# Optimization experiments

Measured on AMD Instinct MI355X. Metric: run time of the kernel, lower is better.

Reference implementation:

```python
import jax, jax.numpy as jnp
import numpy as np

B, S_CTX, S_Q, D_CTX, D_Q = 16, 2048, 2048, 1024, 1024
MASK_P = 0.1  # fraction of masked context positions


def setup_inputs() -> dict:
    key = jax.random.key(0)
    k1, k2, k3, k4 = jax.random.split(key, 4)
    context = jax.random.normal(k1, (B, S_CTX, D_CTX), dtype=jnp.float32)
    query = jax.random.normal(k2, (S_Q, B, D_Q), dtype=jnp.float32)  # [q_steps, batch, query_size]
    W = jax.random.normal(k3, (D_CTX, D_Q), dtype=jnp.float32)       # learned bilinear weights
    context_mask = jax.random.uniform(k4, (B, S_CTX)) < MASK_P       # True = masked position
    return {"context": context, "query": query, "W": W, "context_mask": context_mask}


def reference(context, query, W, context_mask):
    # scores[b, q, s] = context[b, s, :] @ W @ query[q, b, :]   (temp = 1.0, so no scaling)
    cw = jnp.einsum('bsd,de->bse', context, W)            # [B, S_ctx, D_q]
    scores = jnp.einsum('bse,qbe->bqs', cw, query)        # [B, S_q, S_ctx]
    neg = jnp.asarray(-1e30, scores.dtype)                # finite stand-in for -inf (NaN-safe)
    scores = jnp.where(context_mask[:, None, :], neg, scores)
    attn = jax.nn.softmax(scores, axis=2)                 # [B, S_q, S_ctx]
    # rows where the whole context is masked get attention zeroed out
    all_masked = jnp.all(context_mask, axis=1)[:, None, None]
    attn = jnp.where(all_masked, jnp.asarray(0.0, attn.dtype), attn)
    composition = jnp.einsum('bqs,bsd->qbd', attn, context)  # [S_q, B, D_ctx]
    attn_out = attn.transpose(1, 0, 2)                       # [S_q, B, S_ctx]
    return attn_out, composition
```

## Files before the change

kernel.cpp:

```cpp
#include <hip/hip_runtime.h>
#include <cmath>

#define B_  16
#define SEQ 2048
#define DIM 1024
#define LDST 40

typedef short  short8 __attribute__((ext_vector_type(8)));
typedef short  sh4    __attribute__((ext_vector_type(4)));
typedef float  f32x4  __attribute__((ext_vector_type(4)));

__device__ __forceinline__ unsigned short f2bf(float x) {
  unsigned u = __builtin_bit_cast(unsigned, x);
  return (unsigned short)((u + 0x7fffu + ((u >> 16) & 1u)) >> 16);
}
__device__ __forceinline__ float bf2f(unsigned short h) {
  unsigned u = ((unsigned)h) << 16;
  return __builtin_bit_cast(float, u);
}

__device__ __forceinline__ void gl16(const void* g, void* l) {
  __builtin_amdgcn_global_load_lds(
      (const __attribute__((address_space(1))) void*)g,
      (__attribute__((address_space(3))) void*)l, 16, 0, 0);
}

__global__ __launch_bounds__(256) void cvt_ctx(const float* __restrict__ X,
                                               unsigned short* __restrict__ hi,
                                               unsigned short* __restrict__ lo) {
  const size_t N8 = (size_t)B_ * SEQ * DIM / 8;
  for (size_t i = (size_t)blockIdx.x * 256 + threadIdx.x; i < N8;
       i += (size_t)gridDim.x * 256) {
    const size_t base = i * 8;
    float4 a = *(const float4*)&X[base];
    float4 c = *(const float4*)&X[base + 4];
    const float xs[8] = {a.x, a.y, a.z, a.w, c.x, c.y, c.z, c.w};
    short8 h, l;
#pragma unroll
    for (int j = 0; j < 8; ++j) {
      unsigned short hh = f2bf(xs[j]);
      h[j] = (short)hh;
      l[j] = (short)f2bf(xs[j] - bf2f(hh));
    }
    *(short8*)&hi[base] = h;
    *(short8*)&lo[base] = l;
  }
}

__global__ __launch_bounds__(256) void t_ctx(const float* __restrict__ X,
                                             unsigned short* __restrict__ T) {
  __shared__ unsigned short L[64 * 72];
  const int t = threadIdx.x;
  const int d0 = blockIdx.x * 64, s0 = blockIdx.y * 64, b = blockIdx.z;
#pragma unroll
  for (int p = 0; p < 4; ++p) {
    const int sl = (t >> 4) + p * 16, d4 = (t & 15) * 4;
    float4 v = *(const float4*)&X[((size_t)b * SEQ + s0 + sl) * DIM + d0 + d4];
    sh4 o = {(short)f2bf(v.x), (short)f2bf(v.y), (short)f2bf(v.z), (short)f2bf(v.w)};
    *(sh4*)&L[sl * 72 + d4] = o;
  }
  __syncthreads();
#pragma unroll
  for (int p = 0; p < 4; ++p) {
    const int dl = (t >> 4) + p * 16, s4 = (t & 15) * 4;
    sh4 o = {(short)L[(s4 + 0) * 72 + dl], (short)L[(s4 + 1) * 72 + dl],
             (short)L[(s4 + 2) * 72 + dl], (short)L[(s4 + 3) * 72 + dl]};
    *(sh4*)&T[((size_t)b * DIM + d0 + dl) * SEQ + s0 + s4] = o;
  }
}

__global__ __launch_bounds__(256) void g1_z(const float* __restrict__ Q,
                                            const float* __restrict__ W,
                                            unsigned short* __restrict__ zhi,
                                            unsigned short* __restrict__ zlo) {
  __shared__ unsigned short Ah[128 * LDST], Al[128 * LDST];
  __shared__ unsigned short Bh[128 * LDST], Bl[128 * LDST];
  const int tid = threadIdx.x;
  const int m0 = blockIdx.y * 128, n0 = blockIdx.x * 128;
  const int wave = tid >> 6, lane = tid & 63;
  const int wm = (wave >> 1) * 64, wn = (wave & 1) * 64;
  const int rl = tid & 127;

  const float* srow = (tid < 128) ? Q + (size_t)(m0 + rl) * DIM
                                  : W + (size_t)(n0 + rl) * DIM;
  unsigned short* th = (tid < 128) ? Ah : Bh;
  unsigned short* tl = (tid < 128) ? Al : Bl;

  f32x4 acc[4][4];
#pragma unroll
  for (int i = 0; i < 4; ++i)
#pragma unroll
    for (int j = 0; j < 4; ++j) acc[i][j] = (f32x4){0.f, 0.f, 0.f, 0.f};

  for (int kc = 0; kc < DIM; kc += 32) {
    float4 fv[8];
#pragma unroll
    for (int j = 0; j < 8; ++j) fv[j] = *(const float4*)&srow[kc + j * 4];
    __syncthreads();
    short8 hv[4], lv[4];
#pragma unroll
    for (int j = 0; j < 8; ++j) {
      const float x[4] = {fv[j].x, fv[j].y, fv[j].z, fv[j].w};
#pragma unroll
      for (int c = 0; c < 4; ++c) {
        unsigned short h = f2bf(x[c]);
        unsigned short l = f2bf(x[c] - bf2f(h));
        hv[j >> 1][(j & 1) * 4 + c] = (short)h;
        lv[j >> 1][(j & 1) * 4 + c] = (short)l;
      }
    }
#pragma unroll
    for (int j = 0; j < 4; ++j) {
      *(short8*)&th[rl * LDST + j * 8] = hv[j];
      *(short8*)&tl[rl * LDST + j * 8] = lv[j];
    }
    __syncthreads();

    short8 ah[4], al[4], bh[4], bl[4];
#pragma unroll
    for (int f = 0; f < 4; ++f) {
      const int ao = (wm + f * 16 + (lane & 15)) * LDST + (lane >> 4) * 8;
      const int bo = (wn + f * 16 + (lane & 15)) * LDST + (lane >> 4) * 8;
      ah[f] = *(const short8*)&Ah[ao];  al[f] = *(const short8*)&Al[ao];
      bh[f] = *(const short8*)&Bh[bo];  bl[f] = *(const short8*)&Bl[bo];
    }
#pragma unroll
    for (int i = 0; i < 4; ++i)
#pragma unroll
      for (int j = 0; j < 4; ++j) {
        acc[i][j] = __builtin_amdgcn_mfma_f32_16x16x32_bf16(ah[i], bh[j], acc[i][j], 0, 0, 0);
        acc[i][j] = __builtin_amdgcn_mfma_f32_16x16x32_bf16(al[i], bh[j], acc[i][j], 0, 0, 0);
        acc[i][j] = __builtin_amdgcn_mfma_f32_16x16x32_bf16(ah[i], bl[j], acc[i][j], 0, 0, 0);
      }
  }
#pragma unroll
  for (int i = 0; i < 4; ++i)
#pragma unroll
    for (int j = 0; j < 4; ++j)
#pragma unroll
      for (int r = 0; r < 4; ++r) {
        const int row = m0 + wm + i * 16 + (lane >> 4) * 4 + r;
        const int col = n0 + wn + j * 16 + (lane & 15);
        const float v = acc[i][j][r];
        const unsigned short h = f2bf(v);
        zhi[(size_t)row * DIM + col] = h;
        zlo[(size_t)row * DIM + col] = f2bf(v - bf2f(h));
      }
}

#define G2GRID (16 * 16 * B_)
__global__ __launch_bounds__(256) void g2_scores(const unsigned short* __restrict__ zhi,
                                                 const unsigned short* __restrict__ zlo,
                                                 const unsigned short* __restrict__ chi,
                                                 const unsigned short* __restrict__ clo,
                                                 float* __restrict__ Sc) {
  __shared__ unsigned short Sh[128 * 32], Sl[128 * 32];
  __shared__ unsigned short Qh[128 * 32], Ql[128 * 32];
  const int tid = threadIdx.x, lane = tid & 63, wave = tid >> 6;

  const int lin = blockIdx.x;
  const int swz = (lin & 7) * (G2GRID / 8) + (lin >> 3);
  const int s0 = (swz & 15) * 128;
  const int q0 = ((swz >> 4) & 15) * 128;
  const int b  = swz >> 8;

  const int wm = (wave >> 1) * 64;
  const int wn = (wave & 1) * 64;

  const int r_sub = lane >> 2;
  const int c_sub = (((lane & 3) ^ ((lane >> 3) & 3))) * 8;

  f32x4 acc[4][4];
#pragma unroll
  for (int i = 0; i < 4; ++i)
#pragma unroll
    for (int j = 0; j < 4; ++j) acc[i][j] = (f32x4){0.f, 0.f, 0.f, 0.f};

  for (int kc = 0; kc < DIM; kc += 32) {
    if (wave == 0) {
#pragma unroll
      for (int it = 0; it < 8; ++it)
        gl16(&chi[((size_t)b * SEQ + s0 + it * 16 + r_sub) * DIM + kc + c_sub], &Sh[it * 512]);
    } else if (wave == 1) {
#pragma unroll
      for (int it = 0; it < 8; ++it)
        gl16(&clo[((size_t)b * SEQ + s0 + it * 16 + r_sub) * DIM + kc + c_sub], &Sl[it * 512]);
    } else if (wave == 2) {
#pragma unroll
      for (int it = 0; it < 8; ++it)
        gl16(&zhi[((size_t)(q0 + it * 16 + r_sub) * B_ + b) * DIM + kc + c_sub], &Qh[it * 512]);
    } else {
#pragma unroll
      for (int it = 0; it < 8; ++it)
        gl16(&zlo[((size_t)(q0 + it * 16 + r_sub) * B_ + b) * DIM + kc + c_sub], &Ql[it * 512]);
    }
    __syncthreads();

    short8 sh_[4], sl_[4], qh_[4], ql_[4];
#pragma unroll
    for (int f = 0; f < 4; ++f) {
      const int ra = wm + f * 16 + (lane & 15);
      const int rb = wn + f * 16 + (lane & 15);
      const int so = ra * 32 + (((lane >> 4) ^ ((ra >> 1) & 3))) * 8;
      const int qo = rb * 32 + (((lane >> 4) ^ ((rb >> 1) & 3))) * 8;
      sh_[f] = *(const short8*)&Sh[so];  sl_[f] = *(const short8*)&Sl[so];
      qh_[f] = *(const short8*)&Qh[qo];  ql_[f] = *(const short8*)&Ql[qo];
    }
#pragma unroll
    for (int i = 0; i < 4; ++i)
#pragma unroll
      for (int j = 0; j < 4; ++j) {
        acc[i][j] = __builtin_amdgcn_mfma_f32_16x16x32_bf16(sh_[i], qh_[j], acc[i][j], 0, 0, 0);
        acc[i][j] = __builtin_amdgcn_mfma_f32_16x16x32_bf16(sl_[i], qh_[j], acc[i][j], 0, 0, 0);
        acc[i][j] = __builtin_amdgcn_mfma_f32_16x16x32_bf16(sh_[i], ql_[j], acc[i][j], 0, 0, 0);
      }
    __syncthreads();
  }

#pragma unroll
  for (int i = 0; i < 4; ++i)
#pragma unroll
    for (int j = 0; j < 4; ++j) {
      const int s = s0 + wm + i * 16 + (lane >> 4) * 4;
      const int q = q0 + wn + j * 16 + (lane & 15);
      f32x4 v = {acc[i][j][0], acc[i][j][1], acc[i][j][2], acc[i][j][3]};
      __builtin_nontemporal_store(v, (f32x4*)&Sc[((size_t)q * B_ + b) * SEQ + s]);
    }
}

__global__ __launch_bounds__(256) void kernel_softmax(float* __restrict__ attn,
                                                      const int* __restrict__ mask) {
  const int row = blockIdx.x;
  const int b = row & (B_ - 1);
  float* p = attn + (size_t)row * SEQ;
  const int* m = mask + (size_t)b * SEQ;
  const int t = threadIdx.x;

  float v[8];
  float mx = -INFINITY;
#pragma unroll
  for (int i = 0; i < 8; ++i) {
    const int s = t + i * 256;
    float x = p[s];
    x = m[s] ? -1e30f : x;
    v[i] = x;
    mx = fmaxf(mx, x);
  }
#pragma unroll
  for (int off = 32; off > 0; off >>= 1) mx = fmaxf(mx, __shfl_xor(mx, off));
  __shared__ float redmax[4];
  __shared__ float redsum[4];
  if ((t & 63) == 0) redmax[t >> 6] = mx;
  __syncthreads();
  mx = fmaxf(fmaxf(redmax[0], redmax[1]), fmaxf(redmax[2], redmax[3]));

  float sum = 0.f;
#pragma unroll
  for (int i = 0; i < 8; ++i) {
    v[i] = __expf(v[i] - mx);
    sum += v[i];
  }
#pragma unroll
  for (int off = 32; off > 0; off >>= 1) sum += __shfl_xor(sum, off);
  if ((t & 63) == 0) redsum[t >> 6] = sum;
  __syncthreads();
  sum = (redsum[0] + redsum[1]) + (redsum[2] + redsum[3]);

  const bool allmasked = (mx < -1e29f);
  const float inv = allmasked ? 0.f : 1.f / sum;
#pragma unroll
  for (int i = 0; i < 8; ++i) p[t + i * 256] = v[i] * inv;
}

__global__ __launch_bounds__(256) void g3_comp(const float* __restrict__ attn,
                                               const unsigned short* __restrict__ ctxT,
                                               float* __restrict__ Out) {
  __shared__ unsigned short Ad[128 * 32];
  __shared__ unsigned short Bq[128 * 32];
  const int tid = threadIdx.x, lane = tid & 63, wave = tid >> 6;
  const int b = blockIdx.z;
  const int d0 = blockIdx.x * 128, q0 = blockIdx.y * 128;
  const int wm = (wave >> 1) * 64;
  const int wn = (wave & 1) * 64;

  const int r_sub = lane >> 2;
  const int c_sub = (((lane & 3) ^ ((lane >> 3) & 3))) * 8;

  const int qrow = tid >> 1, shalf = (tid & 1) * 16;
  const float* arow = attn + ((size_t)(q0 + qrow) * B_ + b) * SEQ;
  const int qsw = (qrow >> 1) & 3;
  const int blk_base = (tid & 1) * 2;
  unsigned short* bdst0 = &Bq[qrow * 32 + ((blk_base + 0) ^ qsw) * 8];
  unsigned short* bdst1 = &Bq[qrow * 32 + ((blk_base + 1) ^ qsw) * 8];

  f32x4 acc[4][4];
#pragma unroll
  for (int i = 0; i < 4; ++i)
#pragma unroll
    for (int j = 0; j < 4; ++j) acc[i][j] = (f32x4){0.f, 0.f, 0.f, 0.f};

  for (int kc = 0; kc < SEQ; kc += 32) {
    float4 fv[4];
#pragma unroll
    for (int j = 0; j < 4; ++j) fv[j] = *(const float4*)&arow[kc + shalf + j * 4];
#pragma unroll
    for (int i = 0; i < 2; ++i) {
      const int rb = wave * 32 + i * 16;
      gl16(&ctxT[((size_t)b * DIM + d0 + rb + r_sub) * SEQ + kc + c_sub], &Ad[rb * 32]);
    }
    short8 bv0, bv1;
#pragma unroll
    for (int j = 0; j < 4; ++j) {
      const float x[4] = {fv[j].x, fv[j].y, fv[j].z, fv[j].w};
#pragma unroll
      for (int c = 0; c < 4; ++c) {
        const int e = j * 4 + c;
        if (e < 8) bv0[e] = (short)f2bf(x[c]);
        else       bv1[e - 8] = (short)f2bf(x[c]);
      }
    }
    *(short8*)bdst0 = bv0;
    *(short8*)bdst1 = bv1;
    __syncthreads();

    short8 af[4], bf_[4];
#pragma unroll
    for (int f = 0; f < 4; ++f) {
      const int ra = wm + f * 16 + (lane & 15);
      const int rb = wn + f * 16 + (lane & 15);
      af[f]  = *(const short8*)&Ad[ra * 32 + (((lane >> 4) ^ ((ra >> 1) & 3))) * 8];
      bf_[f] = *(const short8*)&Bq[rb * 32 + (((lane >> 4) ^ ((rb >> 1) & 3))) * 8];
    }
#pragma unroll
    for (int i = 0; i < 4; ++i)
#pragma unroll
      for (int j = 0; j < 4; ++j)
        acc[i][j] = __builtin_amdgcn_mfma_f32_16x16x32_bf16(af[i], bf_[j], acc[i][j], 0, 0, 0);
    __syncthreads();
  }

#pragma unroll
  for (int i = 0; i < 4; ++i)
#pragma unroll
    for (int j = 0; j < 4; ++j) {
      const int d = d0 + wm + i * 16 + (lane >> 4) * 4;
      const int q = q0 + wn + j * 16 + (lane & 15);
      f32x4 v = {acc[i][j][0], acc[i][j][1], acc[i][j][2], acc[i][j][3]};
      __builtin_nontemporal_store(v, (f32x4*)&Out[((size_t)q * B_ + b) * DIM + d]);
    }
}

extern "C" void kernel_launch(void* const* d_in, const int* in_sizes, int n_in,
                              void* d_out, int out_size, void* d_ws, size_t ws_size,
                              hipStream_t stream) {
  const float* context = (const float*)d_in[0];
  const float* query   = (const float*)d_in[1];
  const float* W       = (const float*)d_in[2];
  const int*   mask    = (const int*)d_in[3];

  float* attn = (float*)d_out;
  float* comp = attn + (size_t)SEQ * B_ * SEQ;

  unsigned short* chi = (unsigned short*)comp;
  unsigned short* clo = chi + (size_t)B_ * SEQ * DIM;

  unsigned short* zhi  = (unsigned short*)d_ws;
  unsigned short* zlo  = zhi + (size_t)SEQ * B_ * DIM;
  unsigned short* ctxT = (unsigned short*)d_ws;

  cvt_ctx<<<dim3(4096), 256, 0, stream>>>(context, chi, clo);
  g1_z<<<dim3(DIM / 128, (SEQ * B_) / 128), 256, 0, stream>>>(query, W, zhi, zlo);
  g2_scores<<<dim3(G2GRID), 256, 0, stream>>>(zhi, zlo, chi, clo, attn);
  t_ctx<<<dim3(DIM / 64, SEQ / 64, B_), 256, 0, stream>>>(context, ctxT);
  kernel_softmax<<<dim3(SEQ * B_), 256, 0, stream>>>(attn, mask);
  g3_comp<<<dim3(DIM / 128, SEQ / 128, B_), 256, 0, stream>>>(attn, ctxT, comp);
}
```

Baseline: 1.258 ms.

## Widen composition K-tile to 64, vectorize softmax, transpose from bf16 hi buffer

The composition GEMM now stages a 64-wide K slice per iteration with an 8-way XOR swizzle, which halves the number of barrier-separated iterations and doubles the MFMAs issued per sync. The softmax kernel switches from strided scalar accesses to contiguous float4/int4 loads and stores per thread. The context transpose now reads the already converted bf16 hi buffer instead of the fp32 context, which halves its read traffic and drops the conversion. In exchange, LDS use per block doubles, register pressure rises, and the transpose depends on chi still being intact when it runs.

New measurement: 1.308 ms. +4.0%, slower.

```diff
diff --git a/kernel.cpp b/kernel.cpp
--- a/kernel.cpp
+++ b/kernel.cpp
@@ -47,26 +47,26 @@
   }
 }
 
-__global__ __launch_bounds__(256) void t_ctx(const float* __restrict__ X,
+__global__ __launch_bounds__(256) void t_chi(const unsigned short* __restrict__ H,
                                              unsigned short* __restrict__ T) {
-  __shared__ unsigned short L[64 * 72];
+  __shared__ unsigned short L[64][72];
   const int t = threadIdx.x;
   const int d0 = blockIdx.x * 64, s0 = blockIdx.y * 64, b = blockIdx.z;
-#pragma unroll
-  for (int p = 0; p < 4; ++p) {
-    const int sl = (t >> 4) + p * 16, d4 = (t & 15) * 4;
-    float4 v = *(const float4*)&X[((size_t)b * SEQ + s0 + sl) * DIM + d0 + d4];
-    sh4 o = {(short)f2bf(v.x), (short)f2bf(v.y), (short)f2bf(v.z), (short)f2bf(v.w)};
-    *(sh4*)&L[sl * 72 + d4] = o;
-  }
+  const int sl = t >> 2, dp = (t & 3) * 16;
+  short8 v0 = *(const short8*)&H[((size_t)b * SEQ + s0 + sl) * DIM + d0 + dp];
+  short8 v1 = *(const short8*)&H[((size_t)b * SEQ + s0 + sl) * DIM + d0 + dp + 8];
+  *(short8*)&L[sl][dp] = v0;
+  *(short8*)&L[sl][dp + 8] = v1;
   __syncthreads();
-#pragma unroll
-  for (int p = 0; p < 4; ++p) {
-    const int dl = (t >> 4) + p * 16, s4 = (t & 15) * 4;
-    sh4 o = {(short)L[(s4 + 0) * 72 + dl], (short)L[(s4 + 1) * 72 + dl],
-             (short)L[(s4 + 2) * 72 + dl], (short)L[(s4 + 3) * 72 + dl]};
-    *(sh4*)&T[((size_t)b * DIM + d0 + dl) * SEQ + s0 + s4] = o;
-  }
+  const int dl = t >> 2, sp = (t & 3) * 16;
+  short8 o0, o1;
+#pragma unroll
+  for (int k = 0; k < 8; ++k) {
+    o0[k] = (short)L[sp + k][dl];
+    o1[k] = (short)L[sp + 8 + k][dl];
+  }
+  *(short8*)&T[((size_t)b * DIM + d0 + dl) * SEQ + s0 + sp] = o0;
+  *(short8*)&T[((size_t)b * DIM + d0 + dl) * SEQ + s0 + sp + 8] = o1;
 }
 
 __global__ __launch_bounds__(256) void g1_z(const float* __restrict__ Q,
@@ -236,16 +236,17 @@
   const int* m = mask + (size_t)b * SEQ;
   const int t = threadIdx.x;
 
-  float v[8];
+  float4 va = *(const float4*)&p[t * 8];
+  float4 vb = *(const float4*)&p[t * 8 + 4];
+  int4 ma = *(const int4*)&m[t * 8];
+  int4 mb = *(const int4*)&m[t * 8 + 4];
+  float v[8] = {ma.x ? -1e30f : va.x, ma.y ? -1e30f : va.y,
+                ma.z ? -1e30f : va.z, ma.w ? -1e30f : va.w,
+                mb.x ? -1e30f : vb.x, mb.y ? -1e30f : vb.y,
+                mb.z ? -1e30f : vb.z, mb.w ? -1e30f : vb.w};
   float mx = -INFINITY;
 #pragma unroll
-  for (int i = 0; i < 8; ++i) {
-    const int s = t + i * 256;
-    float x = p[s];
-    x = m[s] ? -1e30f : x;
-    v[i] = x;
-    mx = fmaxf(mx, x);
-  }
+  for (int i = 0; i < 8; ++i) mx = fmaxf(mx, v[i]);
 #pragma unroll
   for (int off = 32; off > 0; off >>= 1) mx = fmaxf(mx, __shfl_xor(mx, off));
   __shared__ float redmax[4];
@@ -268,30 +269,31 @@
 
   const bool allmasked = (mx < -1e29f);
   const float inv = allmasked ? 0.f : 1.f / sum;
-#pragma unroll
-  for (int i = 0; i < 8; ++i) p[t + i * 256] = v[i] * inv;
+  float4 oa = {v[0] * inv, v[1] * inv, v[2] * inv, v[3] * inv};
+  float4 ob = {v[4] * inv, v[5] * inv, v[6] * inv, v[7] * inv};
+  *(float4*)&p[t * 8] = oa;
+  *(float4*)&p[t * 8 + 4] = ob;
 }
 
 __global__ __launch_bounds__(256) void g3_comp(const float* __restrict__ attn,
                                                const unsigned short* __restrict__ ctxT,
                                                float* __restrict__ Out) {
-  __shared__ unsigned short Ad[128 * 32];
-  __shared__ unsigned short Bq[128 * 32];
+  __shared__ unsigned short Ad[128 * 64];
+  __shared__ unsigned short Bq[128 * 64];
   const int tid = threadIdx.x, lane = tid & 63, wave = tid >> 6;
   const int b = blockIdx.z;
   const int d0 = blockIdx.x * 128, q0 = blockIdx.y * 128;
   const int wm = (wave >> 1) * 64;
   const int wn = (wave & 1) * 64;
 
-  const int r_sub = lane >> 2;
-  const int c_sub = (((lane & 3) ^ ((lane >> 3) & 3))) * 8;
-
-  const int qrow = tid >> 1, shalf = (tid & 1) * 16;
-  const float* arow = attn + ((size_t)(q0 + qrow) * B_ + b) * SEQ;
-  const int qsw = (qrow >> 1) & 3;
-  const int blk_base = (tid & 1) * 2;
-  unsigned short* bdst0 = &Bq[qrow * 32 + ((blk_base + 0) ^ qsw) * 8];
-  unsigned short* bdst1 = &Bq[qrow * 32 + ((blk_base + 1) ^ qsw) * 8];
+  const int r8 = lane >> 3;
+  const int c8 = lane & 7;
+  const unsigned short* agp =
+      ctxT + ((size_t)b * DIM + d0 + wave * 32 + r8) * SEQ + (size_t)((c8 ^ r8) * 8);
+
+  const int qrow = tid >> 1;
+  const int rk = qrow & 7;
+  const float* arow = attn + ((size_t)(q0 + qrow) * B_ + b) * SEQ + (tid & 1) * 32;
 
   f32x4 acc[4][4];
 #pragma unroll
@@ -299,43 +301,46 @@
 #pragma unroll
     for (int j = 0; j < 4; ++j) acc[i][j] = (f32x4){0.f, 0.f, 0.f, 0.f};
 
-  for (int kc = 0; kc < SEQ; kc += 32) {
-    float4 fv[4];
-#pragma unroll
-    for (int j = 0; j < 4; ++j) fv[j] = *(const float4*)&arow[kc + shalf + j * 4];
-#pragma unroll
-    for (int i = 0; i < 2; ++i) {
-      const int rb = wave * 32 + i * 16;
-      gl16(&ctxT[((size_t)b * DIM + d0 + rb + r_sub) * SEQ + kc + c_sub], &Ad[rb * 32]);
-    }
-    short8 bv0, bv1;
-#pragma unroll
-    for (int j = 0; j < 4; ++j) {
-      const float x[4] = {fv[j].x, fv[j].y, fv[j].z, fv[j].w};
-#pragma unroll
-      for (int c = 0; c < 4; ++c) {
-        const int e = j * 4 + c;
-        if (e < 8) bv0[e] = (short)f2bf(x[c]);
-        else       bv1[e - 8] = (short)f2bf(x[c]);
-      }
-    }
-    *(short8*)bdst0 = bv0;
-    *(short8*)bdst1 = bv1;
-    __syncthreads();
-
-    short8 af[4], bf_[4];
+  for (int kc = 0; kc < SEQ; kc += 64) {
+    float4 fv[8];
+#pragma unroll
+    for (int jj = 0; jj < 8; ++jj) fv[jj] = *(const float4*)&arow[kc + jj * 4];
+#pragma unroll
+    for (int g = 0; g < 4; ++g)
+      gl16(agp + (size_t)g * 8 * SEQ + kc, &Ad[(wave * 32 + g * 8) * 64]);
+#pragma unroll
+    for (int jw = 0; jw < 4; ++jw) {
+      short8 w;
+#pragma unroll
+      for (int e = 0; e < 8; ++e) {
+        const float4 f4 = fv[jw * 2 + (e >> 2)];
+        const float x = (e & 3) == 0 ? f4.x : (e & 3) == 1 ? f4.y : (e & 3) == 2 ? f4.z : f4.w;
+        w[e] = (short)f2bf(x);
+      }
+      const int blk = (tid & 1) * 4 + jw;
+      *(short8*)&Bq[qrow * 64 + ((blk ^ rk)) * 8] = w;
+    }
+    __syncthreads();
+
+    short8 af[4][2], bf_[4][2];
 #pragma unroll
     for (int f = 0; f < 4; ++f) {
       const int ra = wm + f * 16 + (lane & 15);
       const int rb = wn + f * 16 + (lane & 15);
-      af[f]  = *(const short8*)&Ad[ra * 32 + (((lane >> 4) ^ ((ra >> 1) & 3))) * 8];
-      bf_[f] = *(const short8*)&Bq[rb * 32 + (((lane >> 4) ^ ((rb >> 1) & 3))) * 8];
+#pragma unroll
+      for (int h = 0; h < 2; ++h) {
+        const int kbA = h * 4 + (lane >> 4);
+        af[f][h]  = *(const short8*)&Ad[ra * 64 + ((kbA ^ (ra & 7))) * 8];
+        bf_[f][h] = *(const short8*)&Bq[rb * 64 + ((kbA ^ (rb & 7))) * 8];
+      }
     }
 #pragma unroll
     for (int i = 0; i < 4; ++i)
 #pragma unroll
-      for (int j = 0; j < 4; ++j)
-        acc[i][j] = __builtin_amdgcn_mfma_f32_16x16x32_bf16(af[i], bf_[j], acc[i][j], 0, 0, 0);
+      for (int j = 0; j < 4; ++j) {
+        acc[i][j] = __builtin_amdgcn_mfma_f32_16x16x32_bf16(af[i][0], bf_[j][0], acc[i][j], 0, 0, 0);
+        acc[i][j] = __builtin_amdgcn_mfma_f32_16x16x32_bf16(af[i][1], bf_[j][1], acc[i][j], 0, 0, 0);
+      }
     __syncthreads();
   }
 
@@ -371,7 +376,7 @@
   cvt_ctx<<<dim3(4096), 256, 0, stream>>>(context, chi, clo);
   g1_z<<<dim3(DIM / 128, (SEQ * B_) / 128), 256, 0, stream>>>(query, W, zhi, zlo);
   g2_scores<<<dim3(G2GRID), 256, 0, stream>>>(zhi, zlo, chi, clo, attn);
-  t_ctx<<<dim3(DIM / 64, SEQ / 64, B_), 256, 0, stream>>>(context, ctxT);
+  t_chi<<<dim3(DIM / 64, SEQ / 64, B_), 256, 0, stream>>>(chi, ctxT);
   kernel_softmax<<<dim3(SEQ * B_), 256, 0, stream>>>(attn, mask);
   g3_comp<<<dim3(DIM / 128, SEQ / 128, B_), 256, 0, stream>>>(attn, ctxT, comp);
 }
```
